# Kernel tuning notes

Measured on AMD Instinct MI355X. Metric: run time of the kernel, lower is better.

Reference implementation:

```python
import jax, jax.numpy as jnp
import numpy as np

B, S, D_IN, D_OUT, H = 4, 2048, 1024, 1024, 16
HD = D_OUT // H

def setup_inputs() -> dict:
    key = jax.random.key(0)
    ks = jax.random.split(key, 6)
    s = 1.0 / np.sqrt(D_IN)
    return {
        "x": jax.random.normal(ks[0], (B, S, D_IN), dtype=jnp.float32),
        "Wq": jax.random.uniform(ks[1], (D_IN, D_OUT), jnp.float32, -s, s),
        "Wk": jax.random.uniform(ks[2], (D_IN, D_OUT), jnp.float32, -s, s),
        "Wv": jax.random.uniform(ks[3], (D_IN, D_OUT), jnp.float32, -s, s),
        "Wo": jax.random.uniform(ks[4], (D_OUT, D_OUT), jnp.float32, -s, s),
        "bo": jax.random.uniform(ks[5], (D_OUT,), jnp.float32, -s, s),
    }

def reference(x, Wq, Wk, Wv, Wo, bo):
    b, n, _ = x.shape
    # project and split heads: [b, h, n, hd]
    q = (x @ Wq).reshape(b, n, H, HD).transpose(0, 2, 1, 3)
    k = (x @ Wk).reshape(b, n, H, HD).transpose(0, 2, 1, 3)
    v = (x @ Wv).reshape(b, n, H, HD).transpose(0, 2, 1, 3)
    scores = jnp.einsum("bhqd,bhkd->bhqk", q, k) / np.sqrt(HD).astype(np.float32)
    causal = jnp.tril(jnp.ones((n, n), dtype=bool))
    scores = jnp.where(causal, scores, -jnp.inf)
    attn = jax.nn.softmax(scores, axis=-1)  # dropout p=0.0 -> identity
    ctx = jnp.einsum("bhqk,bhkd->bhqd", attn, v)
    ctx = ctx.transpose(0, 2, 1, 3).reshape(b, n, D_OUT)
    return ctx @ Wo + bo
```

## Files before the change

kernel.cpp:

```cpp
#include <hip/hip_runtime.h>
#include <stdint.h>

#define B_   4
#define S_   2048
#define DI   1024
#define DOUT 1024
#define NHD  16
#define HD   64

typedef __attribute__((ext_vector_type(8))) short short8;
typedef __attribute__((ext_vector_type(4))) float f32x4;
typedef __attribute__((ext_vector_type(16))) float f32x16;

__device__ __forceinline__ unsigned short f32_bf16(float f) {
  union { float f; unsigned u; } v; v.f = f;
  unsigned r = v.u + 0x7FFFu + ((v.u >> 16) & 1u);
  return (unsigned short)(r >> 16);
}

__device__ __forceinline__ unsigned cvt_pk_bf16(float a, float b) {
  unsigned r;
  asm("v_cvt_pk_bf16_f32 %0, %1, %2" : "=v"(r) : "v"(a), "v"(b));
  return r;
}

__device__ __forceinline__ void pl32swap(unsigned &dst, unsigned &src) {
  asm("v_permlane32_swap_b32 %0, %1" : "+v"(dst), "+v"(src));
}

__device__ __forceinline__ float max3f(float a, float b, float c) {
  float d;
  asm("v_max3_f32 %0, %1, %2, %3" : "=v"(d) : "v"(a), "v"(b), "v"(c));
  return d;
}

__device__ __forceinline__ void gl_lds16(const void* g, void* s) {
  __builtin_amdgcn_global_load_lds(
      (const __attribute__((address_space(1))) unsigned int*)g,
      (__attribute__((address_space(3))) unsigned int*)s, 16, 0, 0);
}

#define EXP2(x) __builtin_amdgcn_exp2f(x)

__global__ __launch_bounds__(256) void cvt_kernel(const float* __restrict__ src,
                                                  unsigned short* __restrict__ dst, int n4) {
  int i = blockIdx.x * blockDim.x + threadIdx.x;
  if (i < n4) {
    float4 v = ((const float4*)src)[i];
    ushort4 o;
    o.x = f32_bf16(v.x); o.y = f32_bf16(v.y); o.z = f32_bf16(v.z); o.w = f32_bf16(v.w);
    ((ushort4*)dst)[i] = o;
  }
}

__global__ __launch_bounds__(256) void wtrans4_kernel(
    const float* __restrict__ W0, const float* __restrict__ W1,
    const float* __restrict__ W2, const float* __restrict__ W3,
    unsigned short* __restrict__ T0, unsigned short* __restrict__ T1,
    unsigned short* __restrict__ T2, unsigned short* __restrict__ T3) {
  __shared__ __attribute__((aligned(16))) float tile[64][65];
  const int z = blockIdx.z;
  const float* W = z == 0 ? W0 : z == 1 ? W1 : z == 2 ? W2 : W3;
  unsigned short* Wt = z == 0 ? T0 : z == 1 ? T1 : z == 2 ? T2 : T3;
  const int k0 = blockIdx.y * 64;
  const int n0 = blockIdx.x * 64;
  const int tid = threadIdx.x;
#pragma unroll
  for (int i = 0; i < 4; i++) {
    int c = tid + i * 256;
    int r = c >> 4;
    int cc = (c & 15) * 4;
    float4 v = *(const float4*)(W + (size_t)(k0 + r) * DOUT + n0 + cc);
    tile[r][cc] = v.x; tile[r][cc + 1] = v.y; tile[r][cc + 2] = v.z; tile[r][cc + 3] = v.w;
  }
  __syncthreads();
#pragma unroll
  for (int i = 0; i < 4; i++) {
    int c = tid + i * 256;
    int r = c >> 4;
    int cc = (c & 15) * 4;
    ushort4 o;
    o.x = f32_bf16(tile[cc + 0][r]);
    o.y = f32_bf16(tile[cc + 1][r]);
    o.z = f32_bf16(tile[cc + 2][r]);
    o.w = f32_bf16(tile[cc + 3][r]);
    *(ushort4*)(Wt + (size_t)(n0 + r) * DI + k0 + cc) = o;
  }
}

__device__ __forceinline__ int cswz(int r, int c) {
  return r * 128 + ((((c >> 3) ^ ((r >> 3) & 15)) << 3) | (c & 7));
}

template <int MODE>
__global__ __launch_bounds__(256) void gemm_kernel(
    const unsigned short* __restrict__ A,
    const unsigned short* __restrict__ Bt,
    unsigned short* __restrict__ oQ,
    unsigned short* __restrict__ oK,
    unsigned short* __restrict__ oV,
    float* __restrict__ outF,
    const float* __restrict__ bias,
    int M, int N, int K) {
  __shared__ __attribute__((aligned(16))) unsigned short smem[16384];
  const int tid = threadIdx.x;
  const int lane = tid & 63;
  const int w = tid >> 6;
  const int wm = w >> 1, wn = w & 1;
  const int quad = lane >> 4, l16 = lane & 15;

  const int bid = blockIdx.y * 64 + blockIdx.x;
  const int xcd = bid & 7;
  const int rr = bid >> 3;
  const int bx = xcd * 8 + (rr & 7);
  const int by = rr >> 3;
  const int m0 = bx * 128;
  const int n0 = by * 128;

  const int lr = lane >> 2;
  const int lc8 = (lane & 3) * 8;
  const unsigned short* gA0 = A + (size_t)(m0 + w * 32 + lr) * K + lc8;
  const unsigned short* gA1 = gA0 + (size_t)16 * K;
  const unsigned short* gB0 = Bt + (size_t)(n0 + w * 32 + lr) * K + lc8;
  const unsigned short* gB1 = gB0 + (size_t)16 * K;
  const int sA0o = (w * 2 + 0) * 512;
  const int sA1o = (w * 2 + 1) * 512;
  const int sB0o = 4096 + (w * 2 + 0) * 512;
  const int sB1o = 4096 + (w * 2 + 1) * 512;

  f32x4 acc[4][4] = {};

  gl_lds16(gA0, smem + sA0o);
  gl_lds16(gA1, smem + sA1o);
  gl_lds16(gB0, smem + sB0o);
  gl_lds16(gB1, smem + sB1o);
  __syncthreads();

  for (int k0 = 0; k0 < K; k0 += 32) {
    const int cb = ((k0 >> 5) & 1) << 13;
    const int nb = 8192 - cb;
    if (k0 + 32 < K) {
      gl_lds16(gA0 + k0 + 32, smem + nb + sA0o);
      gl_lds16(gA1 + k0 + 32, smem + nb + sA1o);
      gl_lds16(gB0 + k0 + 32, smem + nb + sB0o);
      gl_lds16(gB1 + k0 + 32, smem + nb + sB1o);
    }
    short8 af[4], bfr[4];
#pragma unroll
    for (int mi = 0; mi < 4; mi++)
      af[mi] = *(const short8*)(smem + cb + (wm * 64 + mi * 16 + l16) * 32 + quad * 8);
#pragma unroll
    for (int ni = 0; ni < 4; ni++)
      bfr[ni] = *(const short8*)(smem + cb + 4096 + (wn * 64 + ni * 16 + l16) * 32 + quad * 8);
#pragma unroll
    for (int mi = 0; mi < 4; mi++)
#pragma unroll
      for (int ni = 0; ni < 4; ni++)
        acc[mi][ni] = __builtin_amdgcn_mfma_f32_16x16x32_bf16(af[mi], bfr[ni], acc[mi][ni], 0, 0, 0);
    __syncthreads();
  }

  if (MODE == 0) {
    const int which = n0 >> 10;
    if (which == 2) {
#pragma unroll
      for (int mi = 0; mi < 4; mi++)
#pragma unroll
        for (int ni = 0; ni < 4; ni++)
#pragma unroll
          for (int r = 0; r < 4; r++)
            smem[cswz(wm * 64 + mi * 16 + quad * 4 + r, wn * 64 + ni * 16 + l16)] =
                f32_bf16(acc[mi][ni][r]);
      __syncthreads();
      const int b = m0 >> 11, sb = m0 & 2047;
#pragma unroll
      for (int i = 0; i < 8; i++) {
        int c = tid + i * 256;
        int cl = c >> 4;
        int sc = (c & 15) * 8;
        int col = n0 + cl;
        int hh = (col >> 6) & 15, hd = col & 63;
        union { unsigned short u[8]; uint4 v; } t;
#pragma unroll
        for (int jx = 0; jx < 8; jx++) t.u[jx] = smem[cswz(sc + jx, cl)];
        *(uint4*)(oV + (((size_t)(b * NHD + hh)) * HD + hd) * S_ + sb + sc) = t.v;
      }
    } else {
      unsigned short* dst0 = which == 0 ? oQ : oK;
#pragma unroll
      for (int mi = 0; mi < 4; mi++)
#pragma unroll
        for (int ni = 0; ni < 4; ni++) {
          const int col = n0 + wn * 64 + ni * 16 + l16;
          const int hh = (col >> 6) & 15, hd = col & 63;
#pragma unroll
          for (int r = 0; r < 4; r++) {
            const int row = m0 + wm * 64 + mi * 16 + quad * 4 + r;
            int b = row >> 11, s = row & 2047;
            dst0[(((size_t)(b * NHD + hh)) * S_ + s) * HD + hd] = f32_bf16(acc[mi][ni][r]);
          }
        }
    }
  } else {
#pragma unroll
    for (int mi = 0; mi < 4; mi++)
#pragma unroll
      for (int ni = 0; ni < 4; ni++) {
        const int col = n0 + wn * 64 + ni * 16 + l16;
        float bv = bias[col];
#pragma unroll
        for (int r = 0; r < 4; r++) {
          const int row = m0 + wm * 64 + mi * 16 + quad * 4 + r;
          outF[(size_t)row * N + col] = acc[mi][ni][r] + bv;
        }
      }
  }
}

__global__ __launch_bounds__(256, 2) void attn_kernel(
    const unsigned short* __restrict__ Q,
    const unsigned short* __restrict__ Kmat,
    const unsigned short* __restrict__ Vt,
    unsigned short* __restrict__ ctx) {
  __shared__ __attribute__((aligned(16))) unsigned short smem[16384];

  const int tid = threadIdx.x;
  const int lane = tid & 63;
  const int w = tid >> 6;
  const int l32 = lane & 31;
  const int h = lane >> 5;

  const int bid = blockIdx.x;
  const int bh = (bid & 7) * 8 + ((bid >> 3) & 7);
  const int jj = bid >> 6;

  const unsigned short* Qh = Q + (size_t)bh * S_ * HD;
  const unsigned short* Kh = Kmat + (size_t)bh * S_ * HD;
  const unsigned short* Vh = Vt + (size_t)bh * HD * S_;

  const int r1 = tid >> 3, c1 = tid & 7;
  const int sj1 = c1 ^ (r1 & 7);
  const unsigned short* gK1 = Kh + (size_t)r1 * HD + sj1 * 8;
  const unsigned short* gV1 = Vh + (size_t)r1 * S_ + sj1 * 8;
  const int swz = (l32 & 7);

  unsigned short* myP = smem + (size_t)(w * 32) * 72;
  const float scl = 0.18033688f;
  const int b = bh >> 4, head = bh & 15;

#define ASTAGE(t, bf)                                                       \
  do {                                                                      \
    const unsigned short* k_ = gK1 + (size_t)(t) * 64 * HD;                 \
    const unsigned short* v_ = gV1 + (size_t)(t) * 64;                      \
    gl_lds16(k_, smem + (bf) * 4096 + w * 512);                             \
    gl_lds16(k_ + 32 * HD, smem + (bf) * 4096 + 2048 + w * 512);            \
    gl_lds16(v_, smem + 8192 + (bf) * 4096 + w * 512);                      \
    gl_lds16(v_ + (size_t)32 * S_, smem + 8192 + (bf) * 4096 + 2048 + w * 512); \
  } while (0)

  for (int ph = 0; ph < 2; ph++) {
    const int qc = (ph == 0) ? (jj * 8 + w) : (63 - jj * 8 - w);
    const int nt = (qc >> 1) + 1;
    const int ntmax = (ph == 0) ? (jj * 4 + 2) : (32 - jj * 4);
    const int qrow = qc * 32 + l32;

    short8 qf[4];
#pragma unroll
    for (int ks = 0; ks < 4; ks++)
      qf[ks] = *(const short8*)(Qh + (size_t)qrow * HD + ks * 16 + h * 8);

    ASTAGE(0, 0);
    __syncthreads();

    f32x16 oacc[2] = {};
    float m_run = -__builtin_inff();
    float l_run = 0.f;

    for (int kt = 0; kt < ntmax; kt++) {
      if (kt + 1 < ntmax) ASTAGE(kt + 1, (kt + 1) & 1);

      const unsigned short* Kb_ = smem + ((kt & 1) << 12);
      const unsigned short* Vb_ = smem + 8192 + ((kt & 1) << 12);

      if (kt < nt) {
        const int k0 = kt * 64;
        f32x16 sacc[2] = {};
#pragma unroll
        for (int ks = 0; ks < 4; ks++)
#pragma unroll
          for (int mi = 0; mi < 2; mi++) {
            short8 kf = *(const short8*)(Kb_ + (mi * 32 + l32) * 64 + (((ks * 2 + h) ^ swz) << 3));
            sacc[mi] = __builtin_amdgcn_mfma_f32_32x32x16_bf16(kf, qf[ks], sacc[mi], 0, 0, 0);
          }

        if (kt == nt - 1) {
#pragma unroll
          for (int mi = 0; mi < 2; mi++)
#pragma unroll
            for (int e = 0; e < 16; e++) {
              int key = k0 + mi * 32 + (e & 3) + 8 * (e >> 2) + 4 * h;
              if (key > qrow) sacc[mi][e] = -__builtin_inff();
            }
        }
        float vmax = fmaxf(sacc[0][0], sacc[0][1]);
#pragma unroll
        for (int e = 2; e < 16; e += 2) vmax = max3f(vmax, sacc[0][e], sacc[0][e + 1]);
#pragma unroll
        for (int e = 0; e < 16; e += 2) vmax = max3f(vmax, sacc[1][e], sacc[1][e + 1]);
        vmax = fmaxf(vmax, __shfl_xor(vmax, 32));
        const float pm = vmax * scl;
        if (!__all(pm <= m_run + 8.f)) {
          const float mnew = fmaxf(m_run, pm);
          const float alpha = EXP2(m_run - mnew);
          m_run = mnew;
          l_run *= alpha;
#pragma unroll
          for (int mi = 0; mi < 2; mi++) oacc[mi] *= alpha;
        }

        float rs = 0.f;
#pragma unroll
        for (int mi = 0; mi < 2; mi++)
#pragma unroll
          for (int e = 0; e < 16; e++) {
            float p = EXP2(fmaf(sacc[mi][e], scl, -m_run));
            sacc[mi][e] = p;
            rs += p;
          }
        rs += __shfl_xor(rs, 32);
        l_run += rs;

        short8 pfr[4];
#pragma unroll
        for (int mi = 0; mi < 2; mi++) {
          unsigned w0 = cvt_pk_bf16(sacc[mi][0], sacc[mi][1]);
          unsigned w1 = cvt_pk_bf16(sacc[mi][2], sacc[mi][3]);
          unsigned w2 = cvt_pk_bf16(sacc[mi][4], sacc[mi][5]);
          unsigned w3 = cvt_pk_bf16(sacc[mi][6], sacc[mi][7]);
          pl32swap(w0, w2);
          pl32swap(w1, w3);
          union { unsigned u[4]; short8 s; } lo;
          lo.u[0] = w0; lo.u[1] = w1; lo.u[2] = w2; lo.u[3] = w3;
          pfr[2 * mi + 0] = lo.s;
          unsigned x0 = cvt_pk_bf16(sacc[mi][8], sacc[mi][9]);
          unsigned x1 = cvt_pk_bf16(sacc[mi][10], sacc[mi][11]);
          unsigned x2 = cvt_pk_bf16(sacc[mi][12], sacc[mi][13]);
          unsigned x3 = cvt_pk_bf16(sacc[mi][14], sacc[mi][15]);
          pl32swap(x0, x2);
          pl32swap(x1, x3);
          union { unsigned u[4]; short8 s; } hi;
          hi.u[0] = x0; hi.u[1] = x1; hi.u[2] = x2; hi.u[3] = x3;
          pfr[2 * mi + 1] = hi.s;
        }

#pragma unroll
        for (int ks2 = 0; ks2 < 4; ks2++) {
#pragma unroll
          for (int mi2 = 0; mi2 < 2; mi2++) {
            short8 vf = *(const short8*)(Vb_ + (mi2 * 32 + l32) * 64 + (((ks2 * 2 + h) ^ swz) << 3));
            oacc[mi2] = __builtin_amdgcn_mfma_f32_32x32x16_bf16(vf, pfr[ks2], oacc[mi2], 0, 0, 0);
          }
        }
      }

      __syncthreads();
    }

    const float inv = 1.f / l_run;
#pragma unroll
    for (int mi2 = 0; mi2 < 2; mi2++)
#pragma unroll
      for (int g = 0; g < 4; g++) {
        uint2 pk;
        pk.x = cvt_pk_bf16(oacc[mi2][4 * g + 0] * inv, oacc[mi2][4 * g + 1] * inv);
        pk.y = cvt_pk_bf16(oacc[mi2][4 * g + 2] * inv, oacc[mi2][4 * g + 3] * inv);
        *(uint2*)(myP + l32 * 72 + mi2 * 32 + g * 8 + h * 4) = pk;
      }
#pragma unroll
    for (int p = 0; p < 4; p++) {
      int r = p * 8 + (lane >> 3);
      int c = (lane & 7) * 8;
      uint4 vv = *(const uint4*)(myP + r * 72 + c);
      *(uint4*)(ctx + ((size_t)(b * S_ + qc * 32 + r)) * DOUT + head * 64 + c) = vv;
    }
    __syncthreads();
  }
#undef ASTAGE
}

extern "C" void kernel_launch(void* const* d_in, const int* in_sizes, int n_in,
                              void* d_out, int out_size, void* d_ws, size_t ws_size,
                              hipStream_t stream) {
  const float* x  = (const float*)d_in[0];
  const float* Wq = (const float*)d_in[1];
  const float* Wk = (const float*)d_in[2];
  const float* Wv = (const float*)d_in[3];
  const float* Wo = (const float*)d_in[4];
  const float* bo = (const float*)d_in[5];
  float* out = (float*)d_out;
  char* ws = (char*)d_ws;

  const size_t MB = 1024 * 1024;
  unsigned short* Wqt = (unsigned short*)(ws + 0 * MB);
  unsigned short* Wkt = (unsigned short*)(ws + 2 * MB);
  unsigned short* Wvt = (unsigned short*)(ws + 4 * MB);
  unsigned short* Wot = (unsigned short*)(ws + 6 * MB);
  unsigned short* xb  = (unsigned short*)(ws + 8 * MB);
  unsigned short* Qb  = (unsigned short*)(ws + 24 * MB);
  unsigned short* Kb  = (unsigned short*)(ws + 40 * MB);
  unsigned short* Vtb = (unsigned short*)(ws + 72 * MB);
  unsigned short* ctxb = xb;

  cvt_kernel<<<8192, 256, 0, stream>>>(x, xb, 2097152);
  wtrans4_kernel<<<dim3(16, 16, 4), 256, 0, stream>>>(Wq, Wk, Wv, Wo, Wqt, Wkt, Wvt, Wot);
  gemm_kernel<0><<<dim3(64, 24), 256, 0, stream>>>(xb, Wqt, Qb, Kb, Vtb, nullptr, nullptr,
                                                   8192, 3072, 1024);
  attn_kernel<<<512, 256, 0, stream>>>(Qb, Kb, Vtb, ctxb);
  gemm_kernel<1><<<dim3(64, 8), 256, 0, stream>>>(ctxb, Wot, nullptr, nullptr, nullptr, out, bo,
                                                  8192, 1024, 1024);
}
```

Measured before the change: 236.1 us.

## Triple-buffer GEMM LDS staging with a two-tile-ahead prefetch

Moves the projection GEMM from double buffering to triple buffering in LDS, prefetching two k-tiles ahead. Explicit vmcnt waits replace the full __syncthreads, so global-to-LDS loads overlap more MFMA work and load latency is better hidden. In exchange LDS per block grows from 32KB to 48KB, which may lower occupancy. Each k-step is only 32 wide, so the overlap window is still small.

```diff
diff --git a/kernel.cpp b/kernel.cpp
--- a/kernel.cpp
+++ b/kernel.cpp
@@ -102,7 +102,7 @@
     float* __restrict__ outF,
     const float* __restrict__ bias,
     int M, int N, int K) {
-  __shared__ __attribute__((aligned(16))) unsigned short smem[16384];
+  __shared__ __attribute__((aligned(16))) unsigned short smem[24576];
   const int tid = threadIdx.x;
   const int lane = tid & 63;
   const int w = tid >> 6;
@@ -129,22 +129,25 @@
   const int sB1o = 4096 + (w * 2 + 1) * 512;
 
   f32x4 acc[4][4] = {};
-
-  gl_lds16(gA0, smem + sA0o);
-  gl_lds16(gA1, smem + sA1o);
-  gl_lds16(gB0, smem + sB0o);
-  gl_lds16(gB1, smem + sB1o);
-  __syncthreads();
-
-  for (int k0 = 0; k0 < K; k0 += 32) {
-    const int cb = ((k0 >> 5) & 1) << 13;
-    const int nb = 8192 - cb;
-    if (k0 + 32 < K) {
-      gl_lds16(gA0 + k0 + 32, smem + nb + sA0o);
-      gl_lds16(gA1 + k0 + 32, smem + nb + sA1o);
-      gl_lds16(gB0 + k0 + 32, smem + nb + sB0o);
-      gl_lds16(gB1 + k0 + 32, smem + nb + sB1o);
-    }
+  const int nt = K >> 5;
+
+#define STAGE_T(t, bufS)                                 \
+  do {                                                   \
+    gl_lds16(gA0 + (t) * 32, smem + (bufS) + sA0o);      \
+    gl_lds16(gA1 + (t) * 32, smem + (bufS) + sA1o);      \
+    gl_lds16(gB0 + (t) * 32, smem + (bufS) + sB0o);      \
+    gl_lds16(gB1 + (t) * 32, smem + (bufS) + sB1o);      \
+  } while (0)
+
+  STAGE_T(0, 0);
+  STAGE_T(1, 8192);
+  asm volatile("s_waitcnt vmcnt(4)" ::: "memory");
+  __builtin_amdgcn_s_barrier();
+
+  int cb = 0;
+  for (int it = 0; it < nt; ++it) {
+    const int sb = (cb + 16384 >= 24576) ? (cb - 8192) : (cb + 16384);
+    if (it + 2 < nt) STAGE_T(it + 2, sb);
     short8 af[4], bfr[4];
 #pragma unroll
     for (int mi = 0; mi < 4; mi++)
@@ -157,8 +160,16 @@
 #pragma unroll
       for (int ni = 0; ni < 4; ni++)
         acc[mi][ni] = __builtin_amdgcn_mfma_f32_16x16x32_bf16(af[mi], bfr[ni], acc[mi][ni], 0, 0, 0);
-    __syncthreads();
-  }
+    if (it + 2 < nt) {
+      asm volatile("s_waitcnt vmcnt(4)" ::: "memory");
+    } else {
+      asm volatile("s_waitcnt vmcnt(0)" ::: "memory");
+    }
+    __builtin_amdgcn_s_barrier();
+    cb = (cb + 8192 >= 24576) ? 0 : cb + 8192;
+  }
+#undef STAGE_T
+  __syncthreads();
 
   if (MODE == 0) {
     const int which = n0 >> 10;
@@ -172,7 +183,7 @@
             smem[cswz(wm * 64 + mi * 16 + quad * 4 + r, wn * 64 + ni * 16 + l16)] =
                 f32_bf16(acc[mi][ni][r]);
       __syncthreads();
-      const int b = m0 >> 11, sb = m0 & 2047;
+      const int b = m0 >> 11, sb2 = m0 & 2047;
 #pragma unroll
       for (int i = 0; i < 8; i++) {
         int c = tid + i * 256;
@@ -183,7 +194,7 @@
         union { unsigned short u[8]; uint4 v; } t;
 #pragma unroll
         for (int jx = 0; jx < 8; jx++) t.u[jx] = smem[cswz(sc + jx, cl)];
-        *(uint4*)(oV + (((size_t)(b * NHD + hh)) * HD + hd) * S_ + sb + sc) = t.v;
+        *(uint4*)(oV + (((size_t)(b * NHD + hh)) * HD + hd) * S_ + sb2 + sc) = t.v;
       }
     } else {
       unsigned short* dst0 = which == 0 ? oQ : oK;
```

Result: no change. 237.0 us (+0.4%).
